# Optimization experiments

Measured on AMD Instinct MI355X. Metric: run time of the kernel, lower is better.

Reference implementation:

```python
import jax, jax.numpy as jnp
import numpy as np

B, N = 8, 2048
IN_DIM, MEM_DIM, CTX_DIM = 256, 256, 128

def _linear_params(key, out_dim, in_dim):
    kw, kb = jax.random.split(key)
    bound = 1.0 / np.sqrt(in_dim)
    W = jax.random.uniform(kw, (out_dim, in_dim), jnp.float32, -bound, bound)
    b = jax.random.uniform(kb, (out_dim,), jnp.float32, -bound, bound)
    return W, b

def setup_inputs() -> dict:
    key = jax.random.key(0)
    ks = jax.random.split(key, 8)
    Wq, bq = _linear_params(ks[0], CTX_DIM, IN_DIM)
    Wk, bk = _linear_params(ks[1], CTX_DIM, MEM_DIM)
    Wv, bv = _linear_params(ks[2], MEM_DIM, MEM_DIM)
    Wu, bu = _linear_params(ks[3], MEM_DIM, IN_DIM + MEM_DIM)
    Wr, br = _linear_params(ks[4], MEM_DIM, IN_DIM + MEM_DIM)
    Wc, bc = _linear_params(ks[5], MEM_DIM, IN_DIM + MEM_DIM)
    input_tensor = jax.random.normal(ks[6], (B, N, IN_DIM), jnp.float32)
    previous_memory = jax.random.normal(ks[7], (B, N, MEM_DIM), jnp.float32)
    return dict(input_tensor=input_tensor, previous_memory=previous_memory,
                Wq=Wq, bq=bq, Wk=Wk, bk=bk, Wv=Wv, bv=bv,
                Wu=Wu, bu=bu, Wr=Wr, br=br, Wc=Wc, bc=bc)

def reference(input_tensor, previous_memory, Wq, bq, Wk, bk, Wv, bv, Wu, bu, Wr, br, Wc, bc):
    # QKV projections (torch Linear: y = x @ W.T + b)
    query = jnp.einsum('bnd,cd->bnc', input_tensor, Wq) + bq        # [B,N,CTX]
    key = jnp.einsum('bnm,cm->bnc', previous_memory, Wk) + bk       # [B,N,CTX]
    value = jnp.einsum('bnm,vm->bnv', previous_memory, Wv) + bv     # [B,N,MEM]
    attention_scores = jnp.einsum('bqc,bkc->bqk', query, key)        # [B,N,N]
    attention_probs = jax.nn.softmax(attention_scores, axis=-1)
    context_vector = jnp.einsum('bqk,bkv->bqv', attention_probs, value)  # computed but unused downstream, as in original
    combined = jnp.concatenate([input_tensor, previous_memory], axis=-1)  # [B,N,IN+MEM]
    update_gate = jax.nn.sigmoid(jnp.einsum('bnd,md->bnm', combined, Wu) + bu)
    reset_gate = jax.nn.sigmoid(jnp.einsum('bnd,md->bnm', combined, Wr) + br)
    cand_in = jnp.concatenate([input_tensor, reset_gate * previous_memory], axis=-1)
    candidate_memory = jnp.tanh(jnp.einsum('bnd,md->bnm', cand_in, Wc) + bc)
    new_memory = (1.0 - update_gate) * previous_memory + update_gate * candidate_memory
    return new_memory, attention_probs
```

## Files before the change

kernel.cpp:

```cpp
#include <hip/hip_runtime.h>


typedef _Float16 half8 __attribute__((ext_vector_type(8)));
typedef float floatx4 __attribute__((ext_vector_type(4)));

#define MFMA16(a, b, c) __builtin_amdgcn_mfma_f32_16x16x32_f16((a), (b), (c), 0, 0, 0)

#define OFF_WQH 0
#define OFF_WQL 32768
#define OFF_WKH 65536
#define OFF_WKL 98304
#define OFF_WUH 131072
#define OFF_WRH 262144
#define OFF_WCH 393216
#define OFF_Q   524288
#define OFF_K   2621440
#define OFF_T   4718592
#define OFF_U   8912896

__device__ __forceinline__ void gload16(const void* g, void* l) {
  __builtin_amdgcn_global_load_lds((const __attribute__((address_space(1))) unsigned int*)g,
                                   (__attribute__((address_space(3))) unsigned int*)l, 16, 0, 0);
}

__global__ __launch_bounds__(256) void k0_convert(
    const float* __restrict__ Wq, const float* __restrict__ Wk,
    const float* __restrict__ Wu, const float* __restrict__ Wr,
    const float* __restrict__ Wc, _Float16* __restrict__ ws)
{
  int i = blockIdx.x * 256 + threadIdx.x;
  if (i < 32768) {
    float w = Wq[i];
    _Float16 h = (_Float16)w;
    ws[OFF_WQH + i] = h;
    ws[OFF_WQL + i] = (_Float16)(w - (float)h);
  } else if (i < 65536) {
    int j = i - 32768;
    float w = Wk[j];
    _Float16 h = (_Float16)w;
    ws[OFF_WKH + j] = h;
    ws[OFF_WKL + j] = (_Float16)(w - (float)h);
  } else {
    int j = i - 65536;
    if (j < 131072)      ws[OFF_WUH + j]            = (_Float16)Wu[j];
    else if (j < 262144) ws[OFF_WRH + (j - 131072)] = (_Float16)Wr[j - 131072];
    else                 ws[OFF_WCH + (j - 262144)] = (_Float16)Wc[j - 262144];
  }
}

__global__ __launch_bounds__(512) void k1_proj(
    const float* __restrict__ input, const float* __restrict__ prev,
    const float* __restrict__ bq, const float* __restrict__ bk,
    _Float16* __restrict__ ws)
{
  __shared__ char smem[2 * 8192];
  const int which = blockIdx.y;
  const float* x = which ? prev : input;
  const _Float16* WH = ws + (which ? OFF_WKH : OFF_WQH);
  const _Float16* WL = ws + (which ? OFF_WKL : OFF_WQL);
  const float* bias = which ? bk : bq;
  _Float16* out = ws + (which ? OFF_K : OFF_Q);

  const int tid = threadIdx.x, w = tid >> 6, l = tid & 63;
  const int lr = l & 15, lg = l >> 4;
  const int rows0 = blockIdx.x * 64;
  const int c = w * 16 + lr;

  half8 bh[8], blo[8];
#pragma unroll
  for (int ks = 0; ks < 8; ++ks) {
    bh[ks]  = *(const half8*)(WH + (size_t)c * 256 + ks * 32 + lg * 8);
    blo[ks] = *(const half8*)(WL + (size_t)c * 256 + ks * 32 + lg * 8);
  }
  const float bv = bias[c];

  const int srow = tid >> 5, scol = (tid & 31) * 8;
  const int ssz = (srow & 7) << 4;
  floatx4 st0, st1;

#define K1_LOAD(ch) { const float* src = x + ((size_t)rows0 + (ch) * 16 + srow) * 256 + scol; \
  st0 = *(const floatx4*)src; st1 = *(const floatx4*)(src + 4); }
#define K1_WRITE(ch) { char* bufw = smem + ((ch) & 1) * 8192; \
  half8 h; \
  _Pragma("unroll") for (int j = 0; j < 4; ++j) { \
    h[j] = (_Float16)st0[j]; h[4+j] = (_Float16)st1[j]; } \
  *(half8*)(bufw + srow * 512 + ((scol * 2) ^ ssz)) = h; }

  K1_LOAD(0); K1_WRITE(0);
  __syncthreads();
#pragma unroll 1
  for (int ch = 0; ch < 4; ++ch) {
    if (ch < 3) K1_LOAD(ch + 1);
    const char* buf = smem + (ch & 1) * 8192;
    floatx4 acc = {0.f, 0.f, 0.f, 0.f};
    const int base = lr * 512, sz = (lr & 7) << 4;
#pragma unroll
    for (int ks = 0; ks < 8; ++ks) {
      half8 ah = *(const half8*)(buf + base + ((ks * 64 + lg * 16) ^ sz));
      acc = MFMA16(ah, bh[ks], acc);
      acc = MFMA16(ah, blo[ks], acc);
    }
#pragma unroll
    for (int j = 0; j < 4; ++j)
      out[((size_t)rows0 + ch * 16 + lg * 4 + j) * 128 + c] = (_Float16)(acc[j] + bv);
    if (ch < 3) K1_WRITE(ch + 1);
    __syncthreads();
  }
}

__global__ __launch_bounds__(512) void k2ru(
    const float* __restrict__ input, const float* __restrict__ prev,
    const float* __restrict__ br, const float* __restrict__ bu,
    const _Float16* __restrict__ ws,
    _Float16* __restrict__ t_sc, _Float16* __restrict__ u_sc)
{
  __shared__ char smem[2 * 16384];
  const int tid = threadIdx.x, w = tid >> 6, l = tid & 63;
  const int lr = l & 15, lg = l >> 4;
  const int rows0 = blockIdx.x * 128;
  const int isU = w >> 2;
  const int c = blockIdx.y * 64 + (w & 3) * 16 + lr;

  const _Float16* W = ws + (isU ? OFF_WUH : OFF_WRH);
  half8 bw[16];
#pragma unroll
  for (int ks = 0; ks < 16; ++ks)
    bw[ks] = *(const half8*)(W + (size_t)c * 512 + ks * 32 + lg * 8);
  const float bv = (isU ? bu : br)[c];

  const int srow = tid >> 5, scol = (tid & 31) * 8;
  const int ssz = (srow & 7) << 4;
  floatx4 sI0, sI1, sP0, sP1;

#define K2RU_LOAD(ch) { \
  const float* si = input + ((size_t)rows0 + (ch) * 16 + srow) * 256 + scol; \
  const float* sp = prev  + ((size_t)rows0 + (ch) * 16 + srow) * 256 + scol; \
  sI0 = *(const floatx4*)si; sI1 = *(const floatx4*)(si + 4); \
  sP0 = *(const floatx4*)sp; sP1 = *(const floatx4*)(sp + 4); }
#define K2RU_WRITE(ch) { char* bufw = smem + ((ch) & 1) * 16384; \
  half8 hi, hp; \
  _Pragma("unroll") for (int j = 0; j < 4; ++j) { \
    hi[j] = (_Float16)sI0[j]; hi[4+j] = (_Float16)sI1[j]; \
    hp[j] = (_Float16)sP0[j]; hp[4+j] = (_Float16)sP1[j]; } \
  int o = srow * 1024 + ((scol * 2) ^ ssz); \
  *(half8*)(bufw + o) = hi; *(half8*)(bufw + o + 512) = hp; }

  K2RU_LOAD(0); K2RU_WRITE(0);
  __syncthreads();
#pragma unroll 1
  for (int ch = 0; ch < 8; ++ch) {
    if (ch < 7) K2RU_LOAD(ch + 1);
    const char* buf = smem + (ch & 1) * 16384;
    floatx4 acc = {0.f, 0.f, 0.f, 0.f};
    const int base = lr * 1024, sz = (lr & 7) << 4;
#pragma unroll
    for (int ks = 0; ks < 16; ++ks) {
      half8 a = *(const half8*)(buf + base + ((ks * 64 + lg * 16) ^ sz));
      acc = MFMA16(a, bw[ks], acc);
    }
#pragma unroll
    for (int j = 0; j < 4; ++j) {
      const int crow = lg * 4 + j;
      const size_t grow = (size_t)rows0 + ch * 16 + crow;
      float g = 1.f / (1.f + __expf(-(acc[j] + bv)));
      if (!isU) {
        float m = (float)*(const _Float16*)(buf + crow * 1024 + 512 + ((c * 2) ^ ((crow & 7) << 4)));
        t_sc[grow * 256 + c] = (_Float16)(g * m);
      } else {
        u_sc[grow * 256 + c] = (_Float16)g;
      }
    }
    if (ch < 7) K2RU_WRITE(ch + 1);
    __syncthreads();
  }
}

#define K2C_LOAD(ch) { \
  const float* si = input + ((size_t)rows0 + (ch) * 16 + srow) * 256 + scol; \
  sI0 = *(const floatx4*)si; sI1 = *(const floatx4*)(si + 4); \
  sT = *(const half8*)(t_sc + ((size_t)rows0 + (ch) * 16 + srow) * 256 + scol); }
#define K2C_WRITE(ch) { char* bufw = smemc + ((ch) & 1) * 16384; \
  half8 hi; \
  _Pragma("unroll") for (int j = 0; j < 4; ++j) { hi[j] = (_Float16)sI0[j]; hi[4+j] = (_Float16)sI1[j]; } \
  int o = srow * 1024 + ((scol * 2) ^ ssz); \
  *(half8*)(bufw + o) = hi; *(half8*)(bufw + o + 512) = sT; }

#define K3_STAGE(Kg, dst, ch) { \
  const char* g_ = (Kg) + (ch) * 32768; \
  _Pragma("unroll") for (int i_ = 0; i_ < 4; ++i_) { \
    int o_ = w * 1024 + i_ * 8192 + l * 16; \
    int row_ = o_ >> 8, col_ = o_ & 255; \
    gload16(g_ + row_ * 256 + (col_ ^ ((row_ & 7) << 4)), (dst) + w * 1024 + i_ * 8192); } }

__device__ __forceinline__ void k2c_body(
    char* smemc, int job, int tid,
    const float* __restrict__ input, const float* __restrict__ prev,
    const float* __restrict__ bc, const _Float16* __restrict__ ws,
    const _Float16* __restrict__ t_sc, const _Float16* __restrict__ u_sc,
    float* __restrict__ out0)
{
  const int w = tid >> 6, l = tid & 63;
  const int lr = l & 15, lg = l >> 4;
  const int rows0 = (job & 255) * 64;
  const int c = (job >> 8) * 128 + w * 16 + lr;

  half8 bw[16];
#pragma unroll
  for (int ks = 0; ks < 16; ++ks)
    bw[ks] = *(const half8*)(ws + OFF_WCH + (size_t)c * 512 + ks * 32 + lg * 8);
  const float bv = bc[c];

  const int srow = tid >> 5, scol = (tid & 31) * 8;
  const int ssz = (srow & 7) << 4;
  floatx4 sI0, sI1;
  half8 sT;

  K2C_LOAD(0); K2C_WRITE(0);
  __syncthreads();
#pragma unroll 1
  for (int ch = 0; ch < 4; ++ch) {
    if (ch < 3) K2C_LOAD(ch + 1);
    const char* buf = smemc + (ch & 1) * 16384;
    floatx4 acc = {0.f, 0.f, 0.f, 0.f};
    const int base = lr * 1024, sz = (lr & 7) << 4;
#pragma unroll
    for (int ks = 0; ks < 16; ++ks) {
      half8 a = *(const half8*)(buf + base + ((ks * 64 + lg * 16) ^ sz));
      acc = MFMA16(a, bw[ks], acc);
    }
#pragma unroll
    for (int j = 0; j < 4; ++j) {
      const size_t grow = (size_t)rows0 + ch * 16 + lg * 4 + j;
      float e2 = __expf(2.f * (acc[j] + bv));
      float cg = (e2 - 1.f) / (e2 + 1.f);
      float u = (float)u_sc[grow * 256 + c];
      float m = prev[grow * 256 + c];
      out0[grow * 256 + c] = (1.f - u) * m + u * cg;
    }
    if (ch < 3) K2C_WRITE(ch + 1);
    __syncthreads();
  }
}

__device__ __forceinline__ void k3b_body(
    char* smem, int job, int tid,
    const _Float16* __restrict__ ws, const float* __restrict__ part,
    float* __restrict__ out1)
{
  const int w = tid >> 6, l = tid & 63;
  const int lr = l & 15, lg = l >> 4;
  const int b = job & 7, q0 = ((job >> 3) & 15) * 128, kh = job >> 7;

  const int q = q0 + w * 16 + lr;
  const _Float16* Q = ws + OFF_Q + ((size_t)b * 2048 + q0 + w * 16) * 128;
  const char* Kg = (const char*)(ws + OFF_K + ((size_t)b * 2048 + kh * 512) * 128);

  half8 qf[4];
#pragma unroll
  for (int ks = 0; ks < 4; ++ks)
    qf[ks] = *(const half8*)(Q + (size_t)lr * 128 + ks * 32 + lg * 8);
  const float inv = 1.f / (part[(size_t)(b * 4 + 0) * 2048 + q] +
                           part[(size_t)(b * 4 + 1) * 2048 + q] +
                           part[(size_t)(b * 4 + 2) * 2048 + q] +
                           part[(size_t)(b * 4 + 3) * 2048 + q]);

  char* kbuf0 = smem; char* kbuf1 = smem + 32768;
  K3_STAGE(Kg, kbuf0, 0);
  __syncthreads();

  float* orow = out1 + ((size_t)b * 2048 + q) * 2048 + kh * 512;
#pragma unroll 1
  for (int ch = 0; ch < 4; ++ch) {
    if (ch < 3) K3_STAGE(Kg, ((ch + 1) & 1) ? kbuf1 : kbuf0, ch + 1);
    const char* buf = (ch & 1) ? kbuf1 : kbuf0;
#pragma unroll
    for (int kt = 0; kt < 8; ++kt) {
      const int kk = kt * 16 + lr;
      const int kbase = kk * 256, ksz = (kk & 7) << 4;
      half8 kf[4];
#pragma unroll
      for (int ks = 0; ks < 4; ++ks)
        kf[ks] = *(const half8*)(buf + kbase + ((ks * 64 + lg * 16) ^ ksz));
      floatx4 acc = {0.f, 0.f, 0.f, 0.f};
#pragma unroll
      for (int ks = 0; ks < 4; ++ks) acc = MFMA16(kf[ks], qf[ks], acc);
      floatx4 v;
#pragma unroll
      for (int j = 0; j < 4; ++j) v[j] = __expf(acc[j] - 14.f) * inv;
      *(floatx4*)(orow + ch * 128 + kt * 16 + lg * 4) = v;
    }
    __syncthreads();
  }
}

__global__ __launch_bounds__(512) void k3a_sums(
    const _Float16* __restrict__ ws, float* __restrict__ part)
{
  __shared__ char kbuf[2][32768];
  const int b = blockIdx.x, q0 = blockIdx.y * 128, kh = blockIdx.z;
  const int tid = threadIdx.x, w = tid >> 6, l = tid & 63;
  const int lr = l & 15, lg = l >> 4;

  const _Float16* Q = ws + OFF_Q + ((size_t)b * 2048 + q0 + w * 16) * 128;
  const char* Kg = (const char*)(ws + OFF_K + ((size_t)b * 2048 + kh * 512) * 128);

  half8 qf[4];
#pragma unroll
  for (int ks = 0; ks < 4; ++ks)
    qf[ks] = *(const half8*)(Q + (size_t)lr * 128 + ks * 32 + lg * 8);

  K3_STAGE(Kg, kbuf[0], 0);
  __syncthreads();

  float se = 0.f;
#pragma unroll 1
  for (int ch = 0; ch < 4; ++ch) {
    if (ch < 3) K3_STAGE(Kg, kbuf[(ch + 1) & 1], ch + 1);
    const char* buf = kbuf[ch & 1];
#pragma unroll
    for (int kt = 0; kt < 8; ++kt) {
      const int kk = kt * 16 + lr;
      const int kbase = kk * 256, ksz = (kk & 7) << 4;
      half8 kf[4];
#pragma unroll
      for (int ks = 0; ks < 4; ++ks)
        kf[ks] = *(const half8*)(buf + kbase + ((ks * 64 + lg * 16) ^ ksz));
      floatx4 acc = {0.f, 0.f, 0.f, 0.f};
#pragma unroll
      for (int ks = 0; ks < 4; ++ks) acc = MFMA16(kf[ks], qf[ks], acc);
#pragma unroll
      for (int j = 0; j < 4; ++j) se += __expf(acc[j] - 14.f);
    }
    __syncthreads();
  }
  se += __shfl_xor(se, 16);
  se += __shfl_xor(se, 32);
  if (lg == 0)
    part[((size_t)b * 4 + kh) * 2048 + q0 + w * 16 + lr] = se;
}

__global__ __launch_bounds__(512) void k2c_kernel(
    const float* __restrict__ input, const float* __restrict__ prev,
    const float* __restrict__ bc, const _Float16* __restrict__ ws,
    const _Float16* __restrict__ t_sc, const _Float16* __restrict__ u_sc,
    float* __restrict__ out0)
{
  __shared__ char smemc[2 * 16384];
  k2c_body(smemc, blockIdx.x, threadIdx.x, input, prev, bc, ws, t_sc, u_sc, out0);
}

__global__ __launch_bounds__(512) void k3b_kernel(
    const _Float16* __restrict__ ws, const float* __restrict__ part,
    float* __restrict__ out1)
{
  __shared__ char smem[65536];
  k3b_body(smem, blockIdx.x, threadIdx.x, ws, part, out1);
}

__global__ __launch_bounds__(512, 4) void kD(
    const float* __restrict__ input, const float* __restrict__ prev,
    const float* __restrict__ bc, const _Float16* __restrict__ ws,
    const float* __restrict__ part,
    const _Float16* __restrict__ t_sc, const _Float16* __restrict__ u_sc,
    float* __restrict__ out0, float* __restrict__ out1)
{
  __shared__ char smem[65536];
  const int role = blockIdx.x & 1;
  const int job = blockIdx.x >> 1;
  if (role == 0)
    k3b_body(smem, job, threadIdx.x, ws, part, out1);
  else
    k2c_body(smem, job, threadIdx.x, input, prev, bc, ws, t_sc, u_sc, out0);
}

extern "C" void kernel_launch(void* const* d_in, const int* in_sizes, int n_in,
                              void* d_out, int out_size, void* d_ws, size_t ws_size,
                              hipStream_t stream)
{
  const float* input = (const float*)d_in[0];
  const float* prev  = (const float*)d_in[1];
  const float* Wq = (const float*)d_in[2];
  const float* bq = (const float*)d_in[3];
  const float* Wk = (const float*)d_in[4];
  const float* bk = (const float*)d_in[5];
  const float* Wu = (const float*)d_in[8];
  const float* bu = (const float*)d_in[9];
  const float* Wr = (const float*)d_in[10];
  const float* br = (const float*)d_in[11];
  const float* Wc = (const float*)d_in[12];
  const float* bc = (const float*)d_in[13];

  float* out0 = (float*)d_out;
  float* out1 = out0 + (size_t)8 * 2048 * 256;
  _Float16* ws = (_Float16*)d_ws;

  float* part = (float*)ws;
  const bool big = ws_size >= (size_t)26214400;

  hipLaunchKernelGGL(k0_convert, dim3(1792), dim3(256), 0, stream, Wq, Wk, Wu, Wr, Wc, ws);
  hipLaunchKernelGGL(k1_proj,    dim3(256, 2), dim3(512), 0, stream, input, prev, bq, bk, ws);

  if (big) {
    _Float16* t_sc = ws + OFF_T;
    _Float16* u_sc = ws + OFF_U;
    hipLaunchKernelGGL(k2ru,     dim3(128, 4), dim3(512), 0, stream, input, prev, br, bu, ws, t_sc, u_sc);
    hipLaunchKernelGGL(k3a_sums, dim3(8, 16, 4), dim3(512), 0, stream, ws, part);
    hipLaunchKernelGGL(kD,       dim3(1024), dim3(512), 0, stream,
                       input, prev, bc, ws, part, t_sc, u_sc, out0, out1);
  } else {
    _Float16* t_sc = (_Float16*)out1;
    _Float16* u_sc = (_Float16*)out1 + 4194304;
    hipLaunchKernelGGL(k2ru,       dim3(128, 4), dim3(512), 0, stream, input, prev, br, bu, ws, t_sc, u_sc);
    hipLaunchKernelGGL(k2c_kernel, dim3(512), dim3(512), 0, stream, input, prev, bc, ws, t_sc, u_sc, out0);
    hipLaunchKernelGGL(k3a_sums,   dim3(8, 16, 4), dim3(512), 0, stream, ws, part);
    hipLaunchKernelGGL(k3b_kernel, dim3(512), dim3(512), 0, stream, ws, part, out1);
  }
}
```

Baseline: 106.5 us.

## Merge Q/K projection and reset/update gate kernels into one interleaved launch

Turns the Q/K projection kernel and the reset/update gate kernel into device bodies and runs them together in one kernel, with even and odd blocks taking different roles. Both are 512-block independent workloads, so one 1024-block launch removes a kernel boundary and lets the two workloads overlap on the CUs. The fused kernel declares 32 KB of shared memory and a minimum of 4 blocks per multiprocessor, which may cap registers for the gate body's 16 preloaded weight fragments. The small-workspace path keeps separate launches.

```diff
diff --git a/kernel.cpp b/kernel.cpp
--- a/kernel.cpp
+++ b/kernel.cpp
@@ -48,22 +48,22 @@
   }
 }
 
-__global__ __launch_bounds__(512) void k1_proj(
+__device__ __forceinline__ void k1_body(
+    char* smem, int job, int tid,
     const float* __restrict__ input, const float* __restrict__ prev,
     const float* __restrict__ bq, const float* __restrict__ bk,
     _Float16* __restrict__ ws)
 {
-  __shared__ char smem[2 * 8192];
-  const int which = blockIdx.y;
+  const int which = job >> 8;
   const float* x = which ? prev : input;
   const _Float16* WH = ws + (which ? OFF_WKH : OFF_WQH);
   const _Float16* WL = ws + (which ? OFF_WKL : OFF_WQL);
   const float* bias = which ? bk : bq;
   _Float16* out = ws + (which ? OFF_K : OFF_Q);
 
-  const int tid = threadIdx.x, w = tid >> 6, l = tid & 63;
+  const int w = tid >> 6, l = tid & 63;
   const int lr = l & 15, lg = l >> 4;
-  const int rows0 = blockIdx.x * 64;
+  const int rows0 = (job & 255) * 64;
   const int c = w * 16 + lr;
 
   half8 bh[8], blo[8];
@@ -108,18 +108,18 @@
   }
 }
 
-__global__ __launch_bounds__(512) void k2ru(
+__device__ __forceinline__ void k2ru_body(
+    char* smem, int job, int tid,
     const float* __restrict__ input, const float* __restrict__ prev,
     const float* __restrict__ br, const float* __restrict__ bu,
     const _Float16* __restrict__ ws,
     _Float16* __restrict__ t_sc, _Float16* __restrict__ u_sc)
 {
-  __shared__ char smem[2 * 16384];
-  const int tid = threadIdx.x, w = tid >> 6, l = tid & 63;
+  const int w = tid >> 6, l = tid & 63;
   const int lr = l & 15, lg = l >> 4;
-  const int rows0 = blockIdx.x * 128;
+  const int rows0 = (job & 127) * 128;
   const int isU = w >> 2;
-  const int c = blockIdx.y * 64 + (w & 3) * 16 + lr;
+  const int c = (job >> 7) * 64 + (w & 3) * 16 + lr;
 
   const _Float16* W = ws + (isU ? OFF_WUH : OFF_WRH);
   half8 bw[16];
@@ -339,22 +339,20 @@
     part[((size_t)b * 4 + kh) * 2048 + q0 + w * 16 + lr] = se;
 }
 
-__global__ __launch_bounds__(512) void k2c_kernel(
-    const float* __restrict__ input, const float* __restrict__ prev,
-    const float* __restrict__ bc, const _Float16* __restrict__ ws,
-    const _Float16* __restrict__ t_sc, const _Float16* __restrict__ u_sc,
-    float* __restrict__ out0)
-{
-  __shared__ char smemc[2 * 16384];
-  k2c_body(smemc, blockIdx.x, threadIdx.x, input, prev, bc, ws, t_sc, u_sc, out0);
-}
-
-__global__ __launch_bounds__(512) void k3b_kernel(
-    const _Float16* __restrict__ ws, const float* __restrict__ part,
-    float* __restrict__ out1)
-{
-  __shared__ char smem[65536];
-  k3b_body(smem, blockIdx.x, threadIdx.x, ws, part, out1);
+__global__ __launch_bounds__(512, 4) void kF(
+    const float* __restrict__ input, const float* __restrict__ prev,
+    const float* __restrict__ bq, const float* __restrict__ bk,
+    const float* __restrict__ br, const float* __restrict__ bu,
+    _Float16* __restrict__ ws,
+    _Float16* __restrict__ t_sc, _Float16* __restrict__ u_sc)
+{
+  __shared__ char smem[32768];
+  const int role = blockIdx.x & 1;
+  const int job = blockIdx.x >> 1;
+  if (role == 0)
+    k2ru_body(smem, job, threadIdx.x, input, prev, br, bu, ws, t_sc, u_sc);
+  else
+    k1_body(smem, job, threadIdx.x, input, prev, bq, bk, ws);
 }
 
 __global__ __launch_bounds__(512, 4) void kD(
@@ -371,6 +369,43 @@
     k3b_body(smem, job, threadIdx.x, ws, part, out1);
   else
     k2c_body(smem, job, threadIdx.x, input, prev, bc, ws, t_sc, u_sc, out0);
+}
+
+__global__ __launch_bounds__(512) void k1_kernel(
+    const float* __restrict__ input, const float* __restrict__ prev,
+    const float* __restrict__ bq, const float* __restrict__ bk,
+    _Float16* __restrict__ ws)
+{
+  __shared__ char smem[2 * 8192];
+  k1_body(smem, (blockIdx.y << 8) | blockIdx.x, threadIdx.x, input, prev, bq, bk, ws);
+}
+
+__global__ __launch_bounds__(512) void k2ru_kernel(
+    const float* __restrict__ input, const float* __restrict__ prev,
+    const float* __restrict__ br, const float* __restrict__ bu,
+    const _Float16* __restrict__ ws,
+    _Float16* __restrict__ t_sc, _Float16* __restrict__ u_sc)
+{
+  __shared__ char smem[2 * 16384];
+  k2ru_body(smem, (blockIdx.y << 7) | blockIdx.x, threadIdx.x, input, prev, br, bu, ws, t_sc, u_sc);
+}
+
+__global__ __launch_bounds__(512) void k2c_kernel(
+    const float* __restrict__ input, const float* __restrict__ prev,
+    const float* __restrict__ bc, const _Float16* __restrict__ ws,
+    const _Float16* __restrict__ t_sc, const _Float16* __restrict__ u_sc,
+    float* __restrict__ out0)
+{
+  __shared__ char smemc[2 * 16384];
+  k2c_body(smemc, blockIdx.x, threadIdx.x, input, prev, bc, ws, t_sc, u_sc, out0);
+}
+
+__global__ __launch_bounds__(512) void k3b_kernel(
+    const _Float16* __restrict__ ws, const float* __restrict__ part,
+    float* __restrict__ out1)
+{
+  __shared__ char smem[65536];
+  k3b_body(smem, blockIdx.x, threadIdx.x, ws, part, out1);
 }
 
 extern "C" void kernel_launch(void* const* d_in, const int* in_sizes, int n_in,
@@ -398,21 +433,22 @@
   const bool big = ws_size >= (size_t)26214400;
 
   hipLaunchKernelGGL(k0_convert, dim3(1792), dim3(256), 0, stream, Wq, Wk, Wu, Wr, Wc, ws);
-  hipLaunchKernelGGL(k1_proj,    dim3(256, 2), dim3(512), 0, stream, input, prev, bq, bk, ws);
 
   if (big) {
     _Float16* t_sc = ws + OFF_T;
     _Float16* u_sc = ws + OFF_U;
-    hipLaunchKernelGGL(k2ru,     dim3(128, 4), dim3(512), 0, stream, input, prev, br, bu, ws, t_sc, u_sc);
+    hipLaunchKernelGGL(kF, dim3(1024), dim3(512), 0, stream,
+                       input, prev, bq, bk, br, bu, ws, t_sc, u_sc);
     hipLaunchKernelGGL(k3a_sums, dim3(8, 16, 4), dim3(512), 0, stream, ws, part);
-    hipLaunchKernelGGL(kD,       dim3(1024), dim3(512), 0, stream,
+    hipLaunchKernelGGL(kD, dim3(1024), dim3(512), 0, stream,
                        input, prev, bc, ws, part, t_sc, u_sc, out0, out1);
   } else {
     _Float16* t_sc = (_Float16*)out1;
     _Float16* u_sc = (_Float16*)out1 + 4194304;
-    hipLaunchKernelGGL(k2ru,       dim3(128, 4), dim3(512), 0, stream, input, prev, br, bu, ws, t_sc, u_sc);
-    hipLaunchKernelGGL(k2c_kernel, dim3(512), dim3(512), 0, stream, input, prev, bc, ws, t_sc, u_sc, out0);
-    hipLaunchKernelGGL(k3a_sums,   dim3(8, 16, 4), dim3(512), 0, stream, ws, part);
-    hipLaunchKernelGGL(k3b_kernel, dim3(512), dim3(512), 0, stream, ws, part, out1);
-  }
-}
+    hipLaunchKernelGGL(k1_kernel,   dim3(256, 2), dim3(512), 0, stream, input, prev, bq, bk, ws);
+    hipLaunchKernelGGL(k2ru_kernel, dim3(128, 4), dim3(512), 0, stream, input, prev, br, bu, ws, t_sc, u_sc);
+    hipLaunchKernelGGL(k2c_kernel,  dim3(512), dim3(512), 0, stream, input, prev, bc, ws, t_sc, u_sc, out0);
+    hipLaunchKernelGGL(k3a_sums,    dim3(8, 16, 4), dim3(512), 0, stream, ws, part);
+    hipLaunchKernelGGL(k3b_kernel,  dim3(512), dim3(512), 0, stream, ws, part, out1);
+  }
+}
```

Result: slower. 109.2 us (+2.5%).
